# Optimization experiments

Measured on AMD Instinct MI355X. Metric: run time of the kernel, lower is better.

Reference implementation:

```python
import jax, jax.numpy as jnp
import numpy as np

TEMPERATURE = 0.04


def _d3tod2(t):
    # 'c h w -> (h w) c'
    c, h, w = t.shape
    return jnp.transpose(t, (1, 2, 0)).reshape(h * w, c)


def setup_inputs() -> dict:
    key = jax.random.key(0)
    k1, k2 = jax.random.split(key)
    B, C, H, W = 4, 128, 96, 96
    # scale 0.05 keeps dot/temperature in a numerically sane range for exp
    x = jax.random.normal(k1, (B, C, H, W), dtype=jnp.float32) * 0.05
    label = jax.random.randint(k2, (B, 1, H, W), 0, 3, dtype=jnp.int32)
    return {"x": x, "label": label}


def reference(x, label):
    B, C, H, W = x.shape
    hw = H * W
    feat_1 = _d3tod2(x[0])                     # [HW, C]
    feat_2 = _d3tod2(x[1])                     # [HW, C]
    gt1 = label[0, 0].reshape(hw)              # [HW]
    gt2 = label[1, 0].reshape(hw)              # [HW]
    sim = jnp.exp(jnp.matmul(feat_1, feat_2.T) / TEMPERATURE)  # [HW, HW]
    mask = gt1[:, None] == gt2[None, :]        # [HW, HW] label-equality
    pos_sum = jnp.sum(jnp.where(mask, sim, jnp.zeros((), sim.dtype)))
    total_sum = jnp.sum(sim)
    loss = -jnp.log(pos_sum / total_sum) / (hw * hw)
    return loss
```

## Files before the change

### kernel.cpp

```cpp
#include <hip/hip_runtime.h>
#include <hip/hip_bf16.h>

#define HW 9216
#define CDIM 128
#define ROWS_W 64
#define NCH 12
#define COLS_W (NCH * 16)
#define GRID_I (HW / (ROWS_W * 4))
#define GRID_J (HW / COLS_W)
#define GRID_T (GRID_I * GRID_J)
#define NPART (GRID_T * 4)

using bf16 = __hip_bfloat16;
typedef __attribute__((ext_vector_type(4))) float f32x4;
typedef __attribute__((ext_vector_type(8))) short s16x8;

#define EXP_SCALE 36.067376022224085f

#if __has_builtin(__builtin_amdgcn_exp2f)
#define FEXP2(x) __builtin_amdgcn_exp2f(x)
#else
#define FEXP2(x) exp2f(x)
#endif

__global__ __launch_bounds__(256) void prep_kernel(const float* __restrict__ x,
                                                   bf16* __restrict__ frag) {
    __shared__ float tile[64][65];
    const float* xs = x + (size_t)blockIdx.z * CDIM * HW;
    bf16* fs = frag + (size_t)blockIdx.z * HW * CDIM;
    float scale = (blockIdx.z == 0) ? EXP_SCALE : 1.0f;

    int p0 = blockIdx.x * 64;
    int c0 = blockIdx.y * 64;
    int t  = threadIdx.x;

    int pc = t & 63;
    int cr = t >> 6;
#pragma unroll
    for (int i = 0; i < 16; ++i) {
        int clc = cr + i * 4;
        tile[clc][pc] = xs[(size_t)(c0 + clc) * HW + p0 + pc];
    }
    __syncthreads();

#pragma unroll
    for (int q = 0; q < 2; ++q) {
        int ch   = q * 256 + t;
        int row  = ch & 15;
        int kgq  = (ch >> 4) & 3;
        int ksl  = (ch >> 6) & 1;
        int ib   = (ch >> 7) & 3;
        s16x8 v;
#pragma unroll
        for (int e = 0; e < 8; ++e) {
            __hip_bfloat16 h = __float2bfloat16(tile[ksl * 32 + kgq * 8 + e][ib * 16 + row] * scale);
            v[e] = *reinterpret_cast<short*>(&h);
        }
        size_t chunk = ((size_t)(p0 / 16 + ib) * 4 + (c0 / 32 + ksl)) * 64 + kgq * 16 + row;
        *(s16x8*)(&fs[chunk * 8]) = v;
    }
}

__global__ __launch_bounds__(256, 4) void simsum_kernel(const bf16* __restrict__ frag1,
                                                        const bf16* __restrict__ frag2,
                                                        const int* __restrict__ label,
                                                        float* __restrict__ partials) {
    int t    = threadIdx.x;
    int w    = t >> 6;
    int lane = t & 63;
    int lr   = lane & 15;
    int kg   = lane >> 4;

    int orig = blockIdx.x;
    int wg   = (orig & 7) * (GRID_T / 8) + (orig >> 3);
    int jw   = wg / GRID_I;
    int iw   = wg % GRID_I;

    int r0 = iw * (ROWS_W * 4) + w * ROWS_W;
    int c0 = jw * COLS_W;
    int jb0 = c0 / 16;

    const s16x8* F1 = ((const s16x8*)frag1) + lane;
    const s16x8* F2 = ((const s16x8*)frag2) + lane;

    s16x8 af[4][4];
#pragma unroll
    for (int m = 0; m < 4; ++m)
#pragma unroll
        for (int ks = 0; ks < 4; ++ks)
            af[m][ks] = F1[(size_t)((r0 / 16 + m) * 4 + ks) * 64];

    unsigned pk = 0;
#pragma unroll
    for (int m = 0; m < 4; ++m) {
        int4 v = *(const int4*)(&label[r0 + m * 16 + kg * 4]);
        unsigned b = (unsigned)v.x | ((unsigned)v.y << 2) |
                     ((unsigned)v.z << 4) | ((unsigned)v.w << 6);
        pk |= b << (8 * m);
    }

    const int* lab2 = label + HW;
    float tot = 0.f, pos = 0.f;

    s16x8 bf[4];
#pragma unroll
    for (int ks = 0; ks < 4; ++ks)
        bf[ks] = F2[(size_t)(jb0 * 4 + ks) * 64];

#pragma unroll
    for (int ch = 0; ch < NCH; ++ch) {
        int g2 = lab2[c0 + ch * 16 + lr];
        unsigned d = pk ^ ((unsigned)g2 * 0x55555555u);
        unsigned z = ~(d | (d >> 1)) & 0x55555555u;

        int nb = (ch + 1 < NCH) ? (ch + 1) : 0;
        const s16x8* bnext = F2 + (size_t)((jb0 + nb) * 4) * 64;

        f32x4 acc[4] = {};
#pragma unroll
        for (int ks = 0; ks < 4; ++ks) {
            s16x8 b = bf[ks];
#pragma unroll
            for (int m = 0; m < 4; ++m)
                acc[m] = __builtin_amdgcn_mfma_f32_16x16x32_bf16(af[m][ks], b, acc[m], 0, 0, 0);
            bf[ks] = bnext[(size_t)ks * 64];
        }

#pragma unroll
        for (int m = 0; m < 4; ++m) {
#pragma unroll
            for (int r = 0; r < 4; ++r) {
                float e = FEXP2(acc[m][r]);
                tot += e;
                pos += ((z >> (2 * (m * 4 + r))) & 1u) ? e : 0.f;
            }
        }
    }

#pragma unroll
    for (int off = 32; off; off >>= 1) {
        tot += __shfl_down(tot, off);
        pos += __shfl_down(pos, off);
    }
    if (lane == 0) {
        int wid = orig * 4 + w;
        partials[wid * 2]     = tot;
        partials[wid * 2 + 1] = pos;
    }
}

__global__ __launch_bounds__(256) void finalize_kernel(const float* __restrict__ partials,
                                                       float* __restrict__ out) {
    double tot = 0.0, pos = 0.0;
    int t = threadIdx.x;
    for (int i = t; i < NPART; i += 256) {
        tot += (double)partials[i * 2];
        pos += (double)partials[i * 2 + 1];
    }
#pragma unroll
    for (int off = 32; off; off >>= 1) {
        tot += __shfl_down(tot, off);
        pos += __shfl_down(pos, off);
    }
    __shared__ double rt[4], rp[4];
    int w = t >> 6, lane = t & 63;
    if (lane == 0) { rt[w] = tot; rp[w] = pos; }
    __syncthreads();
    if (t == 0) {
        double T = rt[0] + rt[1] + rt[2] + rt[3];
        double P = rp[0] + rp[1] + rp[2] + rp[3];
        double hw2 = (double)HW * (double)HW;
        out[0] = (float)(-log(P / T) / hw2);
    }
}

extern "C" void kernel_launch(void* const* d_in, const int* in_sizes, int n_in,
                              void* d_out, int out_size, void* d_ws, size_t ws_size,
                              hipStream_t stream) {
    const float* x     = (const float*)d_in[0];
    const int*   label = (const int*)d_in[1];
    float*       out   = (float*)d_out;

    bf16*  frag  = (bf16*)d_ws;
    float* parts = (float*)((char*)d_ws + 2 * (size_t)HW * CDIM * sizeof(bf16));

    dim3 g1(HW / 64, CDIM / 64, 2);
    prep_kernel<<<g1, 256, 0, stream>>>(x, frag);

    simsum_kernel<<<GRID_T, 256, 0, stream>>>(frag, frag + (size_t)HW * CDIM, label, parts);

    finalize_kernel<<<1, 256, 0, stream>>>(parts, out);
}
```

Before: 47.01 us.

## Software-pipeline MFMA clusters with exp epilogue using double-buffered accumulators

Restructures the column-chunk loop so the MFMA cluster for chunk c+1 is issued before the exp/sum epilogue of chunk c. It uses two accumulator sets and two B-fragment prefetch buffers, and raises wave priority around the MFMA blocks. Splitting the running sums into four partial accumulators shortens the dependency chain. The goal is to hide MFMA latency behind the transcendental work, at the cost of more registers, so the occupancy hint drops from 4 to 3 blocks per CU.

```diff
diff --git a/kernel.cpp b/kernel.cpp
--- a/kernel.cpp
+++ b/kernel.cpp
@@ -61,7 +61,7 @@
     }
 }
 
-__global__ __launch_bounds__(256, 4) void simsum_kernel(const bf16* __restrict__ frag1,
+__global__ __launch_bounds__(256, 3) void simsum_kernel(const bf16* __restrict__ frag1,
                                                         const bf16* __restrict__ frag2,
                                                         const int* __restrict__ label,
                                                         float* __restrict__ partials) {
@@ -100,42 +100,73 @@
     }
 
     const int* lab2 = label + HW;
-    float tot = 0.f, pos = 0.f;
-
-    s16x8 bf[4];
-#pragma unroll
-    for (int ks = 0; ks < 4; ++ks)
-        bf[ks] = F2[(size_t)(jb0 * 4 + ks) * 64];
-
-#pragma unroll
-    for (int ch = 0; ch < NCH; ++ch) {
+    float tsum[4] = {0.f, 0.f, 0.f, 0.f};
+    float psum[4] = {0.f, 0.f, 0.f, 0.f};
+
+    s16x8 bP[4], bQ[4];
+#pragma unroll
+    for (int ks = 0; ks < 4; ++ks) {
+        bP[ks] = F2[(size_t)((jb0 + 0) * 4 + ks) * 64];
+        bQ[ks] = F2[(size_t)((jb0 + 1) * 4 + ks) * 64];
+    }
+
+    auto zcalc = [&](int ch) -> unsigned {
         int g2 = lab2[c0 + ch * 16 + lr];
         unsigned d = pk ^ ((unsigned)g2 * 0x55555555u);
-        unsigned z = ~(d | (d >> 1)) & 0x55555555u;
-
-        int nb = (ch + 1 < NCH) ? (ch + 1) : 0;
+        return ~(d | (d >> 1)) & 0x55555555u;
+    };
+
+    auto cluster = [&](int ch, f32x4 (&acc)[4], s16x8 (&buf)[4]) {
+        int nb = (ch + 2 < NCH) ? ch + 2 : ch + 2 - NCH;
         const s16x8* bnext = F2 + (size_t)((jb0 + nb) * 4) * 64;
-
-        f32x4 acc[4] = {};
+#pragma unroll
+        for (int m = 0; m < 4; ++m) acc[m] = f32x4{0.f, 0.f, 0.f, 0.f};
+        __builtin_amdgcn_s_setprio(1);
 #pragma unroll
         for (int ks = 0; ks < 4; ++ks) {
-            s16x8 b = bf[ks];
-#pragma unroll
-            for (int m = 0; m < 4; ++m)
-                acc[m] = __builtin_amdgcn_mfma_f32_16x16x32_bf16(af[m][ks], b, acc[m], 0, 0, 0);
-            bf[ks] = bnext[(size_t)ks * 64];
+            s16x8 b = buf[ks];
+            acc[0] = __builtin_amdgcn_mfma_f32_16x16x32_bf16(af[0][ks], b, acc[0], 0, 0, 0);
+            acc[1] = __builtin_amdgcn_mfma_f32_16x16x32_bf16(af[1][ks], b, acc[1], 0, 0, 0);
+            acc[2] = __builtin_amdgcn_mfma_f32_16x16x32_bf16(af[2][ks], b, acc[2], 0, 0, 0);
+            acc[3] = __builtin_amdgcn_mfma_f32_16x16x32_bf16(af[3][ks], b, acc[3], 0, 0, 0);
+            buf[ks] = bnext[(size_t)ks * 64];
         }
-
+        __builtin_amdgcn_s_setprio(0);
+    };
+
+    auto epi = [&](const f32x4 (&acc)[4], unsigned z) {
 #pragma unroll
         for (int m = 0; m < 4; ++m) {
 #pragma unroll
             for (int r = 0; r < 4; ++r) {
                 float e = FEXP2(acc[m][r]);
-                tot += e;
-                pos += ((z >> (2 * (m * 4 + r))) & 1u) ? e : 0.f;
+                tsum[m] += e;
+                psum[m] += ((z >> (2 * (m * 4 + r))) & 1u) ? e : 0.f;
             }
         }
-    }
+    };
+
+    f32x4 accA[4], accB[4];
+    unsigned zA, zB;
+
+    zA = zcalc(0);
+    cluster(0, accA, bP);
+#pragma unroll
+    for (int c = 1; c <= NCH - 3; c += 2) {
+        zB = zcalc(c);
+        cluster(c, accB, bQ);
+        epi(accA, zA);
+        zA = zcalc(c + 1);
+        cluster(c + 1, accA, bP);
+        epi(accB, zB);
+    }
+    zB = zcalc(NCH - 1);
+    cluster(NCH - 1, accB, bQ);
+    epi(accA, zA);
+    epi(accB, zB);
+
+    float tot = (tsum[0] + tsum[1]) + (tsum[2] + tsum[3]);
+    float pos = (psum[0] + psum[1]) + (psum[2] + psum[3]);
 
 #pragma unroll
     for (int off = 32; off; off >>= 1) {
```

Result: slower. 187.9 us (+299.6%).

## Double per-wave row tile, double-buffer B fragments, vectorize exp accumulation

Applied to the files above, without the earlier changes.

Each wave now covers 128 rows (8 MFMA row blocks) instead of 64, so every loaded B fragment feeds twice as many MFMAs. B fragments are prefetched two chunks ahead through alternating buffers, and MFMA issue is wrapped in raised wave priority. The exp/sum reduction now accumulates into 4-wide vector sums, which shortens the serial dependency chains. In exchange, register pressure roughly doubles (occupancy hint lowered from 4 to 2 blocks), the grid halves, and float summation order changes.

```diff
diff --git a/kernel.cpp b/kernel.cpp
--- a/kernel.cpp
+++ b/kernel.cpp
@@ -3,13 +3,14 @@
 
 #define HW 9216
 #define CDIM 128
-#define ROWS_W 64
+#define ROWS_W 128
 #define NCH 12
 #define COLS_W (NCH * 16)
-#define GRID_I (HW / (ROWS_W * 4))
+#define WPB 4
+#define GRID_I (HW / (ROWS_W * WPB))
 #define GRID_J (HW / COLS_W)
 #define GRID_T (GRID_I * GRID_J)
-#define NPART (GRID_T * 4)
+#define NPART (GRID_T * WPB)
 
 using bf16 = __hip_bfloat16;
 typedef __attribute__((ext_vector_type(4))) float f32x4;
@@ -61,7 +62,7 @@
     }
 }
 
-__global__ __launch_bounds__(256, 4) void simsum_kernel(const bf16* __restrict__ frag1,
+__global__ __launch_bounds__(256, 2) void simsum_kernel(const bf16* __restrict__ frag1,
                                                         const bf16* __restrict__ frag2,
                                                         const int* __restrict__ label,
                                                         float* __restrict__ partials) {
@@ -76,66 +77,89 @@
     int jw   = wg / GRID_I;
     int iw   = wg % GRID_I;
 
-    int r0 = iw * (ROWS_W * 4) + w * ROWS_W;
+    int r0 = iw * (ROWS_W * WPB) + w * ROWS_W;
     int c0 = jw * COLS_W;
     int jb0 = c0 / 16;
 
     const s16x8* F1 = ((const s16x8*)frag1) + lane;
     const s16x8* F2 = ((const s16x8*)frag2) + lane;
 
-    s16x8 af[4][4];
-#pragma unroll
-    for (int m = 0; m < 4; ++m)
+    s16x8 af[8][4];
+#pragma unroll
+    for (int m = 0; m < 8; ++m)
 #pragma unroll
         for (int ks = 0; ks < 4; ++ks)
             af[m][ks] = F1[(size_t)((r0 / 16 + m) * 4 + ks) * 64];
 
-    unsigned pk = 0;
+    unsigned pkA = 0, pkB = 0;
 #pragma unroll
     for (int m = 0; m < 4; ++m) {
-        int4 v = *(const int4*)(&label[r0 + m * 16 + kg * 4]);
-        unsigned b = (unsigned)v.x | ((unsigned)v.y << 2) |
-                     ((unsigned)v.z << 4) | ((unsigned)v.w << 6);
-        pk |= b << (8 * m);
+        int4 va = *(const int4*)(&label[r0 + m * 16 + kg * 4]);
+        pkA |= ((unsigned)va.x | ((unsigned)va.y << 2) |
+                ((unsigned)va.z << 4) | ((unsigned)va.w << 6)) << (8 * m);
+        int4 vb = *(const int4*)(&label[r0 + (m + 4) * 16 + kg * 4]);
+        pkB |= ((unsigned)vb.x | ((unsigned)vb.y << 2) |
+                ((unsigned)vb.z << 4) | ((unsigned)vb.w << 6)) << (8 * m);
     }
 
     const int* lab2 = label + HW;
-    float tot = 0.f, pos = 0.f;
-
-    s16x8 bf[4];
-#pragma unroll
-    for (int ks = 0; ks < 4; ++ks)
-        bf[ks] = F2[(size_t)(jb0 * 4 + ks) * 64];
-
-#pragma unroll
-    for (int ch = 0; ch < NCH; ++ch) {
+    f32x4 tsum = {0.f, 0.f, 0.f, 0.f};
+    f32x4 psum = {0.f, 0.f, 0.f, 0.f};
+
+    s16x8 bP[4], bQ[4];
+#pragma unroll
+    for (int ks = 0; ks < 4; ++ks) {
+        bP[ks] = F2[(size_t)((jb0 + 0) * 4 + ks) * 64];
+        bQ[ks] = F2[(size_t)((jb0 + 1) * 4 + ks) * 64];
+    }
+
+    auto chain = [&](int ch, s16x8 (&buf)[4]) {
         int g2 = lab2[c0 + ch * 16 + lr];
-        unsigned d = pk ^ ((unsigned)g2 * 0x55555555u);
-        unsigned z = ~(d | (d >> 1)) & 0x55555555u;
-
-        int nb = (ch + 1 < NCH) ? (ch + 1) : 0;
+        unsigned g2r = (unsigned)g2 * 0x55555555u;
+        unsigned dA = pkA ^ g2r, dB = pkB ^ g2r;
+        unsigned zA = ~(dA | (dA >> 1)) & 0x55555555u;
+        unsigned zB = ~(dB | (dB >> 1)) & 0x55555555u;
+
+        int nb = (ch + 2 < NCH) ? ch + 2 : ch + 2 - NCH;
         const s16x8* bnext = F2 + (size_t)((jb0 + nb) * 4) * 64;
 
-        f32x4 acc[4] = {};
+        f32x4 acc[8] = {};
+        __builtin_amdgcn_s_setprio(1);
 #pragma unroll
         for (int ks = 0; ks < 4; ++ks) {
-            s16x8 b = bf[ks];
-#pragma unroll
-            for (int m = 0; m < 4; ++m)
+            s16x8 b = buf[ks];
+#pragma unroll
+            for (int m = 0; m < 8; ++m)
                 acc[m] = __builtin_amdgcn_mfma_f32_16x16x32_bf16(af[m][ks], b, acc[m], 0, 0, 0);
-            bf[ks] = bnext[(size_t)ks * 64];
+            buf[ks] = bnext[(size_t)ks * 64];
         }
-
-#pragma unroll
-        for (int m = 0; m < 4; ++m) {
-#pragma unroll
-            for (int r = 0; r < 4; ++r) {
-                float e = FEXP2(acc[m][r]);
-                tot += e;
-                pos += ((z >> (2 * (m * 4 + r))) & 1u) ? e : 0.f;
-            }
+        __builtin_amdgcn_s_setprio(0);
+
+#pragma unroll
+        for (int m = 0; m < 8; ++m) {
+            unsigned z = (m < 4) ? zA : zB;
+            int mb = m & 3;
+            f32x4 ev;
+#pragma unroll
+            for (int r = 0; r < 4; ++r)
+                ev[r] = FEXP2(acc[m][r]);
+            tsum += ev;
+            f32x4 pv;
+#pragma unroll
+            for (int r = 0; r < 4; ++r)
+                pv[r] = ((z >> (2 * (mb * 4 + r))) & 1u) ? ev[r] : 0.f;
+            psum += pv;
         }
-    }
+    };
+
+#pragma unroll
+    for (int c = 0; c < NCH; c += 2) {
+        chain(c,     bP);
+        chain(c + 1, bQ);
+    }
+
+    float tot = (tsum[0] + tsum[1]) + (tsum[2] + tsum[3]);
+    float pos = (psum[0] + psum[1]) + (psum[2] + psum[3]);
 
 #pragma unroll
     for (int off = 32; off; off >>= 1) {
@@ -143,7 +167,7 @@
         pos += __shfl_down(pos, off);
     }
     if (lane == 0) {
-        int wid = orig * 4 + w;
+        int wid = orig * WPB + w;
         partials[wid * 2]     = tot;
         partials[wid * 2 + 1] = pos;
     }
```

Result: no change. 47.51 us (+1.1%).
